# Optimization experiments

Hardware: AMD Instinct MI355X
Metric: run time of the kernel (lower is better)

The kernel has to match this reference:

```python
import jax, jax.numpy as jnp
import numpy as np
import math

B, A, IN_C, OUT_C = 64, 128, 128, 64

def _l2norm(x, eps=1e-12):
    # matches F.normalize(dim=1) on 2D input: x / max(||x||_2, eps) along last dim
    n = jnp.sqrt(jnp.sum(x * x, axis=-1, keepdims=True))
    return x / jnp.maximum(n, eps)

def setup_inputs() -> dict:
    key = jax.random.key(0)
    ks = jax.random.split(key, 7)
    s = 1.0 / math.sqrt(IN_C)
    return {
        "features": jax.random.normal(ks[0], (B, IN_C, A), dtype=jnp.float32),
        "Wq": jax.random.uniform(ks[1], (OUT_C, IN_C), jnp.float32, -s, s),
        "bq": jax.random.uniform(ks[2], (OUT_C,), jnp.float32, -s, s),
        "Wk": jax.random.uniform(ks[3], (OUT_C, IN_C), jnp.float32, -s, s),
        "bk": jax.random.uniform(ks[4], (OUT_C,), jnp.float32, -s, s),
        "Wv": jax.random.uniform(ks[5], (OUT_C, IN_C), jnp.float32, -s, s),
        "bv": jax.random.uniform(ks[6], (OUT_C,), jnp.float32, -s, s),
    }

def reference(features, Wq, bq, Wk, bk, Wv, bv):
    b = features.shape[0]
    f = jnp.transpose(features, (0, 2, 1))          # (b, a, in_c)
    a = f.shape[1]
    q = f @ Wq.T + bq                               # (b, a, d)
    k = f @ Wk.T + bk
    v = f @ Wv.T + bv
    d = q.shape[-1]
    qf = q.reshape(-1, d)                           # (N, d), N = b*a
    kf = k.reshape(-1, d)
    vf = v.reshape(-1, d)
    att = jax.nn.softmax(qf @ kf.T / math.sqrt(d), axis=1)  # (N, N)
    qkv = att @ vf                                  # (N, d)
    qkv_n = _l2norm(qkv).reshape(b, a, d)
    v_n = _l2norm(vf).reshape(b, a, d)
    # sim_s[i,j] = (1/a) * sum_t v_n[i,t] . qkv_n[j,t]  (diagonal-trace over 'a')
    sim_s = jnp.einsum('bad,cad->bc', v_n, qkv_n) / a
    return sim_s
```

## Files before the change

### kernel.cpp

```cpp
#include <hip/hip_runtime.h>
#include <hip/hip_bf16.h>

#define NROW 8192
#define INC  128
#define OUTC 64
#define BG   16

#define QSCALE 0.18033688011112042f

typedef __bf16 bf16x8 __attribute__((ext_vector_type(8)));
typedef __bf16 bf16x4 __attribute__((ext_vector_type(4)));
typedef short  s16x4  __attribute__((ext_vector_type(4)));
typedef float  f32x4  __attribute__((ext_vector_type(4)));

static __device__ __forceinline__ f32x4 mfma16(bf16x8 a, bf16x8 b, f32x4 c) {
    return __builtin_amdgcn_mfma_f32_16x16x32_bf16(a, b, c, 0, 0, 0);
}
static __device__ __forceinline__ f32x4 mfma1k(s16x4 a, s16x4 b, f32x4 c) {
    return __builtin_amdgcn_mfma_f32_16x16x16bf16_1k(a, b, c, 0, 0, 0);
}

static __device__ __forceinline__ bf16x8 cvt8(float4 lo, float4 hi) {
    bf16x8 r;
    r[0] = (__bf16)lo.x; r[1] = (__bf16)lo.y; r[2] = (__bf16)lo.z; r[3] = (__bf16)lo.w;
    r[4] = (__bf16)hi.x; r[5] = (__bf16)hi.y; r[6] = (__bf16)hi.z; r[7] = (__bf16)hi.w;
    return r;
}

__global__ __launch_bounds__(256) void proj_kernel(
    const float* __restrict__ feat,
    const float* __restrict__ Wq, const float* __restrict__ bq,
    const float* __restrict__ Wk, const float* __restrict__ bk,
    const float* __restrict__ Wv, const float* __restrict__ bv,
    __hip_bfloat16* __restrict__ qbf, __hip_bfloat16* __restrict__ kbf,
    __hip_bfloat16* __restrict__ vbf, __hip_bfloat16* __restrict__ vnb)
{
    __shared__ float slab[32 * 132];
    __shared__ float vbuf[32 * 66];
    __shared__ float invb[32];

    const int blk = blockIdx.x;
    const int b   = blk >> 2;
    const int a0  = (blk & 3) * 32;
    const int r0  = b * 128 + a0;
    const float* fb = feat + (size_t)b * INC * 128;

    for (int i = threadIdx.x; i < 32 * 128; i += 256) {
        int c = i >> 5, a = i & 31;
        slab[a * 132 + c] = fb[c * 128 + a0 + a];
    }
    __syncthreads();

    const int w    = threadIdx.x >> 6;
    const int lane = threadIdx.x & 63;
    const int l16  = lane & 15;
    const int quad = lane >> 4;

    f32x4 acc[3][2];
    #pragma unroll
    for (int t = 0; t < 3; ++t)
        #pragma unroll
        for (int u = 0; u < 2; ++u)
            acc[t][u] = (f32x4){0.f, 0.f, 0.f, 0.f};

    #pragma unroll
    for (int kc = 0; kc < 4; ++kc) {
        const int k0 = kc * 32 + quad * 8;
        bf16x8 afr[2];
        #pragma unroll
        for (int u = 0; u < 2; ++u) {
            const float* ar = slab + (u * 16 + l16) * 132 + k0;
            afr[u] = cvt8(*(const float4*)ar, *(const float4*)(ar + 4));
        }
        #pragma unroll
        for (int t = 0; t < 3; ++t) {
            const int tile = w * 3 + t;
            const int mat  = tile >> 2;
            const float* W = (mat == 0) ? Wq : (mat == 1) ? Wk : Wv;
            const float* wr = W + ((tile & 3) * 16 + l16) * INC + k0;
            bf16x8 bfr = cvt8(*(const float4*)wr, *(const float4*)(wr + 4));
            #pragma unroll
            for (int u = 0; u < 2; ++u)
                acc[t][u] = mfma16(afr[u], bfr, acc[t][u]);
        }
    }

    #pragma unroll
    for (int t = 0; t < 3; ++t) {
        const int tile = w * 3 + t;
        const int mat  = tile >> 2;
        const int nt   = tile & 3;
        const float* bias = (mat == 0) ? bq : (mat == 1) ? bk : bv;
        const float bl = bias[nt * 16 + l16];
        if (mat < 2) {
            const float sc = (mat == 0) ? QSCALE : 1.0f;
            __hip_bfloat16* dst = mat ? kbf : qbf;
            #pragma unroll
            for (int u = 0; u < 2; ++u) {
                const int base = ((((r0 >> 4) + u) * 4 + nt) << 8) + l16;
                #pragma unroll
                for (int r = 0; r < 4; ++r)
                    dst[base + (quad * 4 + r) * 16] = __float2bfloat16((acc[t][u][r] + bl) * sc);
            }
        } else {
            #pragma unroll
            for (int u = 0; u < 2; ++u)
                #pragma unroll
                for (int r = 0; r < 4; ++r)
                    vbuf[(u * 16 + quad * 4 + r) * 66 + nt * 16 + l16] = acc[t][u][r] + bl;
        }
    }
    __syncthreads();

    const int rl = threadIdx.x >> 3;
    const int jj = threadIdx.x & 7;
    float ss = 0.f;
    #pragma unroll
    for (int i = 0; i < 8; ++i) {
        float x = vbuf[rl * 66 + jj * 8 + i];
        ss += x * x;
    }
    ss += __shfl_xor(ss, 1, 64);
    ss += __shfl_xor(ss, 2, 64);
    ss += __shfl_xor(ss, 4, 64);
    if (jj == 0) invb[rl] = rsqrtf(fmaxf(ss, 1e-24f));
    __syncthreads();
    float inv = invb[rl];
    bf16x8 vp;
    #pragma unroll
    for (int i = 0; i < 8; ++i)
        vp[i] = (__bf16)(vbuf[rl * 66 + jj * 8 + i] * inv);
    *(bf16x8*)(vnb + (size_t)(r0 + rl) * 64 + jj * 8) = vp;
    const int tl = threadIdx.x & 15;
    const int n  = (threadIdx.x >> 4) & 3;
    const int s_ = threadIdx.x >> 6;
    bf16x8 pack;
    #pragma unroll
    for (int j = 0; j < 8; ++j) {
        int key = s_ * 8 + j;
        pack[j] = (__bf16)(vbuf[key * 66 + n * 16 + tl] * invb[key]);
    }
    const int base = ((((r0 >> 4) + (s_ >> 1)) * 4 + n) << 8) + tl * 16 + (s_ & 1) * 8;
    *(bf16x8*)(vbf + base) = pack;
}

#define ATTN_ITER(K00,K01,K10,K11, NK00,NK01,NK10,NK11,                      \
                  V0,V1,V2,V3,V4,V5,V6,V7,                                   \
                  NV0,NV1,NV2,NV3,NV4,NV5,NV6,NV7)                           \
    do {                                                                     \
        NV0 = *(const s16x4*)(vp);                                           \
        NV1 = *(const s16x4*)(vp + 512);                                     \
        NV2 = *(const s16x4*)(vp + 1024);                                    \
        NV3 = *(const s16x4*)(vp + 1536);                                    \
        NV4 = *(const s16x4*)(vp + 2048);                                    \
        NV5 = *(const s16x4*)(vp + 2560);                                    \
        NV6 = *(const s16x4*)(vp + 3072);                                    \
        NV7 = *(const s16x4*)(vp + 3584);                                    \
        NK00 = *(const bf16x8*)(kp);                                         \
        NK01 = *(const bf16x8*)(kp + 1024);                                  \
        NK10 = *(const bf16x8*)(kp + 2048);                                  \
        NK11 = *(const bf16x8*)(kp + 3072);                                  \
        vp += 4096; kp += 4096;                                              \
        const f32x4 zero = (f32x4){0.f, 0.f, 0.f, 0.f};                      \
        _Pragma("unroll")                                                    \
        for (int u = 0; u < 4; ++u) {                                        \
            f32x4 s0 = mfma16(K00, qf32[u][0], zero);                        \
            s0       = mfma16(K01, qf32[u][1], s0);                          \
            f32x4 s1 = mfma16(K10, qf32[u][0], zero);                        \
            s1       = mfma16(K11, qf32[u][1], s1);                          \
            union { bf16x4 v; s16x4 s; } pf0, pf1;                           \
            _Pragma("unroll")                                                \
            for (int r = 0; r < 4; ++r) {                                    \
                float p0 = __builtin_amdgcn_exp2f(s0[r]);                    \
                float p1 = __builtin_amdgcn_exp2f(s1[r]);                    \
                lp[u] += p0 + p1;                                            \
                pf0.v[r] = (__bf16)p0;                                       \
                pf1.v[r] = (__bf16)p1;                                       \
            }                                                                \
            of[u][0] = mfma1k(pf0.s, V0, of[u][0]);                          \
            of[u][0] = mfma1k(pf1.s, V4, of[u][0]);                          \
            of[u][1] = mfma1k(pf0.s, V1, of[u][1]);                          \
            of[u][1] = mfma1k(pf1.s, V5, of[u][1]);                          \
            of[u][2] = mfma1k(pf0.s, V2, of[u][2]);                          \
            of[u][2] = mfma1k(pf1.s, V6, of[u][2]);                          \
            of[u][3] = mfma1k(pf0.s, V3, of[u][3]);                          \
            of[u][3] = mfma1k(pf1.s, V7, of[u][3]);                          \
        }                                                                    \
    } while (0)

__global__ __launch_bounds__(256, 2) void attn_kernel(
    const __hip_bfloat16* __restrict__ qbf,
    const __hip_bfloat16* __restrict__ kbf,
    const __hip_bfloat16* __restrict__ vbf,
    float* __restrict__ Opart, float* __restrict__ lpart)
{
    const int qb    = blockIdx.x >> 4;
    const int bg    = blockIdx.x & 15;
    const int w     = threadIdx.x >> 6;
    const int lane  = threadIdx.x & 63;
    const int l16   = lane & 15;
    const int quad  = lane >> 4;
    const int r0    = qb * 256 + w * 64;
    const int fo    = l16 * 16 + quad * 4;
    const int fo32  = l16 * 16 + (quad & 1) * 8;
    const int qh    = quad >> 1;

    bf16x8 qf32[4][2];
    #pragma unroll
    for (int u = 0; u < 4; ++u)
        #pragma unroll
        for (int p = 0; p < 2; ++p)
            qf32[u][p] = *(const bf16x8*)(qbf +
                ((((r0 >> 4) + u) * 4 + p * 2 + qh) << 8) + fo32);

    f32x4 of[4][4];
    float lp[4] = {0.f, 0.f, 0.f, 0.f};
    #pragma unroll
    for (int u = 0; u < 4; ++u)
        #pragma unroll
        for (int n = 0; n < 4; ++n)
            of[u][n] = (f32x4){0.f, 0.f, 0.f, 0.f};

    const int ck0 = bg * 32;
    const char* kp = (const char*)kbf + ck0 * 2048 + qh * 512 + fo32 * 2;
    const char* vp = (const char*)vbf + ck0 * 2048 + fo * 2;

    bf16x8 kA00, kA01, kA10, kA11, kB00, kB01, kB10, kB11;
    s16x4  vA0, vA1, vA2, vA3, vA4, vA5, vA6, vA7;
    s16x4  vB0, vB1, vB2, vB3, vB4, vB5, vB6, vB7;

    vA0 = *(const s16x4*)(vp);
    vA1 = *(const s16x4*)(vp + 512);
    vA2 = *(const s16x4*)(vp + 1024);
    vA3 = *(const s16x4*)(vp + 1536);
    vA4 = *(const s16x4*)(vp + 2048);
    vA5 = *(const s16x4*)(vp + 2560);
    vA6 = *(const s16x4*)(vp + 3072);
    vA7 = *(const s16x4*)(vp + 3584);
    kA00 = *(const bf16x8*)(kp);
    kA01 = *(const bf16x8*)(kp + 1024);
    kA10 = *(const bf16x8*)(kp + 2048);
    kA11 = *(const bf16x8*)(kp + 3072);
    vp += 4096; kp += 4096;

    #pragma unroll 1
    for (int body = 0; body < 8; ++body) {
        ATTN_ITER(kA00, kA01, kA10, kA11, kB00, kB01, kB10, kB11,
                  vA0, vA1, vA2, vA3, vA4, vA5, vA6, vA7,
                  vB0, vB1, vB2, vB3, vB4, vB5, vB6, vB7);
        ATTN_ITER(kB00, kB01, kB10, kB11, kA00, kA01, kA10, kA11,
                  vB0, vB1, vB2, vB3, vB4, vB5, vB6, vB7,
                  vA0, vA1, vA2, vA3, vA4, vA5, vA6, vA7);
    }

    #pragma unroll
    for (int u = 0; u < 4; ++u) {
        float v = lp[u];
        v += __shfl_xor(v, 16, 64);
        v += __shfl_xor(v, 32, 64);
        lp[u] = v;
    }

    const int task = (qb * 4 + w) * 16 + bg;
    float* Ob = Opart + (size_t)task * 4096;
    #pragma unroll
    for (int u = 0; u < 4; ++u)
        #pragma unroll
        for (int n = 0; n < 4; ++n)
            #pragma unroll
            for (int r = 0; r < 4; ++r)
                Ob[(u * 16 + quad * 4 + r) * 64 + n * 16 + l16] = of[u][n][r];
    if (quad == 0) {
        #pragma unroll
        for (int u = 0; u < 4; ++u)
            lpart[task * 64 + u * 16 + l16] = lp[u];
    }
}

__global__ __launch_bounds__(256) void combine_kernel(
    const float* __restrict__ Opart, const float* __restrict__ lpart,
    __hip_bfloat16* __restrict__ qnb)
{
    const int r    = blockIdx.x * 4 + (threadIdx.x >> 6);
    const int c    = threadIdx.x & 63;
    const int tile = r >> 6, row = r & 63;
    float acc = 0.f, lsum = 0.f;
    #pragma unroll
    for (int g = 0; g < 16; ++g) {
        int task = tile * 16 + g;
        acc  += Opart[(size_t)task * 4096 + row * 64 + c];
        lsum += lpart[task * 64 + row];
    }
    float q = acc / lsum;
    float ss = q * q;
    ss += __shfl_xor(ss, 1, 64);
    ss += __shfl_xor(ss, 2, 64);
    ss += __shfl_xor(ss, 4, 64);
    ss += __shfl_xor(ss, 8, 64);
    ss += __shfl_xor(ss, 16, 64);
    ss += __shfl_xor(ss, 32, 64);
    qnb[(size_t)r * 64 + c] = __float2bfloat16(q * rsqrtf(fmaxf(ss, 1e-24f)));
}

__global__ __launch_bounds__(256) void sim_kernel(
    const __hip_bfloat16* __restrict__ vnb,
    const __hip_bfloat16* __restrict__ qnb,
    float* __restrict__ out)
{
    const int w    = threadIdx.x >> 6;
    const int lane = threadIdx.x & 63;
    const int l16  = lane & 15;
    const int quad = lane >> 4;
    const int kblk = blockIdx.x * 256;

    f32x4 acc[4][4];
    #pragma unroll
    for (int mi = 0; mi < 4; ++mi)
        #pragma unroll
        for (int ni = 0; ni < 4; ++ni)
            acc[mi][ni] = (f32x4){0.f, 0.f, 0.f, 0.f};

    #pragma unroll
    for (int s = 0; s < 2; ++s) {
        const int ks = w * 2 + s;
        const int k0 = kblk + ks * 32 + quad * 8;
        bf16x8 af[4], bfv[4];
        #pragma unroll
        for (int mi = 0; mi < 4; ++mi)
            af[mi] = *(const bf16x8*)(vnb + (size_t)(mi * 16 + l16) * 8192 + k0);
        #pragma unroll
        for (int ni = 0; ni < 4; ++ni)
            bfv[ni] = *(const bf16x8*)(qnb + (size_t)(ni * 16 + l16) * 8192 + k0);
        #pragma unroll
        for (int mi = 0; mi < 4; ++mi)
            #pragma unroll
            for (int ni = 0; ni < 4; ++ni)
                acc[mi][ni] = mfma16(af[mi], bfv[ni], acc[mi][ni]);
    }

    #pragma unroll
    for (int mi = 0; mi < 4; ++mi)
        #pragma unroll
        for (int ni = 0; ni < 4; ++ni)
            #pragma unroll
            for (int r = 0; r < 4; ++r)
                atomicAdd(&out[(mi * 16 + quad * 4 + r) * 64 + ni * 16 + l16],
                          acc[mi][ni][r] * (1.f / 128.f));
}

extern "C" void kernel_launch(void* const* d_in, const int* in_sizes, int n_in,
                              void* d_out, int out_size, void* d_ws, size_t ws_size,
                              hipStream_t stream)
{
    const float* feat = (const float*)d_in[0];
    const float* Wq   = (const float*)d_in[1];
    const float* bq   = (const float*)d_in[2];
    const float* Wk   = (const float*)d_in[3];
    const float* bk   = (const float*)d_in[4];
    const float* Wv   = (const float*)d_in[5];
    const float* bv   = (const float*)d_in[6];
    float* out = (float*)d_out;

    const size_t MB = 1u << 20;
    char* ws = (char*)d_ws;
    __hip_bfloat16* qbf = (__hip_bfloat16*)(ws);
    __hip_bfloat16* kbf = (__hip_bfloat16*)(ws + 1 * MB);
    __hip_bfloat16* vbf = (__hip_bfloat16*)(ws + 2 * MB);
    __hip_bfloat16* vnb = (__hip_bfloat16*)(ws + 3 * MB);
    float* Opart = (float*)(ws + 4 * MB);
    float* lpart = (float*)(ws + 36 * MB);
    __hip_bfloat16* qnb = (__hip_bfloat16*)(ws + 37 * MB);

    (void)hipMemsetAsync(out, 0, 64 * 64 * sizeof(float), stream);
    proj_kernel<<<256, 256, 0, stream>>>(feat, Wq, bq, Wk, bk, Wv, bv, qbf, kbf, vbf, vnb);
    attn_kernel<<<512, 256, 0, stream>>>(qbf, kbf, vbf, Opart, lpart);
    combine_kernel<<<2048, 256, 0, stream>>>(Opart, lpart, qnb);
    sim_kernel<<<32, 256, 0, stream>>>(vnb, qnb, out);
}
```

Baseline: 121.4 us.

## Widen V fragment loads, fold output zeroing into combine, split sim over more blocks

Changes the V tile layout written by the projection kernel so the attention kernel can fetch each lane's V fragments with four 16-byte loads instead of eight 8-byte loads, halving the load instruction count in the hot loop. Removes the separate hipMemsetAsync by zeroing the output inside the first block of the combine kernel. Doubles the number of sim_kernel blocks, each doing one K-step, to spread the final reduction across more CUs at the cost of twice as many atomic adds.

```diff
diff --git a/kernel.cpp b/kernel.cpp
--- a/kernel.cpp
+++ b/kernel.cpp
@@ -11,6 +11,7 @@
 typedef __bf16 bf16x8 __attribute__((ext_vector_type(8)));
 typedef __bf16 bf16x4 __attribute__((ext_vector_type(4)));
 typedef short  s16x4  __attribute__((ext_vector_type(4)));
+typedef short  s16x8  __attribute__((ext_vector_type(8)));
 typedef float  f32x4  __attribute__((ext_vector_type(4)));
 
 static __device__ __forceinline__ f32x4 mfma16(bf16x8 a, bf16x8 b, f32x4 c) {
@@ -25,6 +26,12 @@
     r[0] = (__bf16)lo.x; r[1] = (__bf16)lo.y; r[2] = (__bf16)lo.z; r[3] = (__bf16)lo.w;
     r[4] = (__bf16)hi.x; r[5] = (__bf16)hi.y; r[6] = (__bf16)hi.z; r[7] = (__bf16)hi.w;
     return r;
+}
+static __device__ __forceinline__ s16x4 vlo(s16x8 x) {
+    return __builtin_shufflevector(x, x, 0, 1, 2, 3);
+}
+static __device__ __forceinline__ s16x4 vhi(s16x8 x) {
+    return __builtin_shufflevector(x, x, 4, 5, 6, 7);
 }
 
 __global__ __launch_bounds__(256) void proj_kernel(
@@ -131,6 +138,7 @@
     for (int i = 0; i < 8; ++i)
         vp[i] = (__bf16)(vbuf[rl * 66 + jj * 8 + i] * inv);
     *(bf16x8*)(vnb + (size_t)(r0 + rl) * 64 + jj * 8) = vp;
+
     const int tl = threadIdx.x & 15;
     const int n  = (threadIdx.x >> 4) & 3;
     const int s_ = threadIdx.x >> 6;
@@ -140,22 +148,21 @@
         int key = s_ * 8 + j;
         pack[j] = (__bf16)(vbuf[key * 66 + n * 16 + tl] * invb[key]);
     }
-    const int base = ((((r0 >> 4) + (s_ >> 1)) * 4 + n) << 8) + tl * 16 + (s_ & 1) * 8;
-    *(bf16x8*)(vbf + base) = pack;
+    const int hblk = (r0 >> 4) + (s_ >> 1);
+    const int eb = hblk * 1024 + (n >> 1) * 512 + tl * 32 + (s_ & 1) * 16 + (n & 1) * 4;
+    bf16x4 plo = __builtin_shufflevector(pack, pack, 0, 1, 2, 3);
+    bf16x4 phi = __builtin_shufflevector(pack, pack, 4, 5, 6, 7);
+    *(bf16x4*)(vbf + eb)     = plo;
+    *(bf16x4*)(vbf + eb + 8) = phi;
 }
 
 #define ATTN_ITER(K00,K01,K10,K11, NK00,NK01,NK10,NK11,                      \
-                  V0,V1,V2,V3,V4,V5,V6,V7,                                   \
-                  NV0,NV1,NV2,NV3,NV4,NV5,NV6,NV7)                           \
+                  W0,W1,W2,W3, NW0,NW1,NW2,NW3)                              \
     do {                                                                     \
-        NV0 = *(const s16x4*)(vp);                                           \
-        NV1 = *(const s16x4*)(vp + 512);                                     \
-        NV2 = *(const s16x4*)(vp + 1024);                                    \
-        NV3 = *(const s16x4*)(vp + 1536);                                    \
-        NV4 = *(const s16x4*)(vp + 2048);                                    \
-        NV5 = *(const s16x4*)(vp + 2560);                                    \
-        NV6 = *(const s16x4*)(vp + 3072);                                    \
-        NV7 = *(const s16x4*)(vp + 3584);                                    \
+        NW0 = *(const s16x8*)(vp);                            \
+        NW1 = *(const s16x8*)(vp + 1024);                     \
+        NW2 = *(const s16x8*)(vp + 2048);                     \
+        NW3 = *(const s16x8*)(vp + 3072);                     \
         NK00 = *(const bf16x8*)(kp);                                         \
         NK01 = *(const bf16x8*)(kp + 1024);                                  \
         NK10 = *(const bf16x8*)(kp + 2048);                                  \
@@ -177,14 +184,14 @@
                 pf0.v[r] = (__bf16)p0;                                       \
                 pf1.v[r] = (__bf16)p1;                                       \
             }                                                                \
-            of[u][0] = mfma1k(pf0.s, V0, of[u][0]);                          \
-            of[u][0] = mfma1k(pf1.s, V4, of[u][0]);                          \
-            of[u][1] = mfma1k(pf0.s, V1, of[u][1]);                          \
-            of[u][1] = mfma1k(pf1.s, V5, of[u][1]);                          \
-            of[u][2] = mfma1k(pf0.s, V2, of[u][2]);                          \
-            of[u][2] = mfma1k(pf1.s, V6, of[u][2]);                          \
-            of[u][3] = mfma1k(pf0.s, V3, of[u][3]);                          \
-            of[u][3] = mfma1k(pf1.s, V7, of[u][3]);                          \
+            of[u][0] = mfma1k(pf0.s, vlo(W0), of[u][0]);                     \
+            of[u][0] = mfma1k(pf1.s, vlo(W2), of[u][0]);                     \
+            of[u][1] = mfma1k(pf0.s, vhi(W0), of[u][1]);                     \
+            of[u][1] = mfma1k(pf1.s, vhi(W2), of[u][1]);                     \
+            of[u][2] = mfma1k(pf0.s, vlo(W1), of[u][2]);                     \
+            of[u][2] = mfma1k(pf1.s, vlo(W3), of[u][2]);                     \
+            of[u][3] = mfma1k(pf0.s, vhi(W1), of[u][3]);                     \
+            of[u][3] = mfma1k(pf1.s, vhi(W3), of[u][3]);                     \
         }                                                                    \
     } while (0)
 
@@ -201,7 +208,6 @@
     const int l16   = lane & 15;
     const int quad  = lane >> 4;
     const int r0    = qb * 256 + w * 64;
-    const int fo    = l16 * 16 + quad * 4;
     const int fo32  = l16 * 16 + (quad & 1) * 8;
     const int qh    = quad >> 1;
 
@@ -223,20 +229,15 @@
 
     const int ck0 = bg * 32;
     const char* kp = (const char*)kbf + ck0 * 2048 + qh * 512 + fo32 * 2;
-    const char* vp = (const char*)vbf + ck0 * 2048 + fo * 2;
+    const char* vp = (const char*)vbf + ck0 * 2048 + l16 * 64 + quad * 16;
 
     bf16x8 kA00, kA01, kA10, kA11, kB00, kB01, kB10, kB11;
-    s16x4  vA0, vA1, vA2, vA3, vA4, vA5, vA6, vA7;
-    s16x4  vB0, vB1, vB2, vB3, vB4, vB5, vB6, vB7;
-
-    vA0 = *(const s16x4*)(vp);
-    vA1 = *(const s16x4*)(vp + 512);
-    vA2 = *(const s16x4*)(vp + 1024);
-    vA3 = *(const s16x4*)(vp + 1536);
-    vA4 = *(const s16x4*)(vp + 2048);
-    vA5 = *(const s16x4*)(vp + 2560);
-    vA6 = *(const s16x4*)(vp + 3072);
-    vA7 = *(const s16x4*)(vp + 3584);
+    s16x8  wA0, wA1, wA2, wA3, wB0, wB1, wB2, wB3;
+
+    wA0 = *(const s16x8*)(vp);
+    wA1 = *(const s16x8*)(vp + 1024);
+    wA2 = *(const s16x8*)(vp + 2048);
+    wA3 = *(const s16x8*)(vp + 3072);
     kA00 = *(const bf16x8*)(kp);
     kA01 = *(const bf16x8*)(kp + 1024);
     kA10 = *(const bf16x8*)(kp + 2048);
@@ -246,11 +247,9 @@
     #pragma unroll 1
     for (int body = 0; body < 8; ++body) {
         ATTN_ITER(kA00, kA01, kA10, kA11, kB00, kB01, kB10, kB11,
-                  vA0, vA1, vA2, vA3, vA4, vA5, vA6, vA7,
-                  vB0, vB1, vB2, vB3, vB4, vB5, vB6, vB7);
+                  wA0, wA1, wA2, wA3, wB0, wB1, wB2, wB3);
         ATTN_ITER(kB00, kB01, kB10, kB11, kA00, kA01, kA10, kA11,
-                  vB0, vB1, vB2, vB3, vB4, vB5, vB6, vB7,
-                  vA0, vA1, vA2, vA3, vA4, vA5, vA6, vA7);
+                  wB0, wB1, wB2, wB3, wA0, wA1, wA2, wA3);
     }
 
     #pragma unroll
@@ -279,8 +278,14 @@
 
 __global__ __launch_bounds__(256) void combine_kernel(
     const float* __restrict__ Opart, const float* __restrict__ lpart,
-    __hip_bfloat16* __restrict__ qnb)
-{
+    __hip_bfloat16* __restrict__ qnb, float* __restrict__ outz)
+{
+    if (blockIdx.x == 0) {
+        #pragma unroll
+        for (int z = 0; z < 4; ++z)
+            ((float4*)outz)[threadIdx.x * 4 + z] = (float4){0.f, 0.f, 0.f, 0.f};
+    }
+
     const int r    = blockIdx.x * 4 + (threadIdx.x >> 6);
     const int c    = threadIdx.x & 63;
     const int tile = r >> 6, row = r & 63;
@@ -311,7 +316,7 @@
     const int lane = threadIdx.x & 63;
     const int l16  = lane & 15;
     const int quad = lane >> 4;
-    const int kblk = blockIdx.x * 256;
+    const int k0   = blockIdx.x * 128 + w * 32 + quad * 8;
 
     f32x4 acc[4][4];
     #pragma unroll
@@ -320,23 +325,18 @@
         for (int ni = 0; ni < 4; ++ni)
             acc[mi][ni] = (f32x4){0.f, 0.f, 0.f, 0.f};
 
-    #pragma unroll
-    for (int s = 0; s < 2; ++s) {
-        const int ks = w * 2 + s;
-        const int k0 = kblk + ks * 32 + quad * 8;
-        bf16x8 af[4], bfv[4];
-        #pragma unroll
-        for (int mi = 0; mi < 4; ++mi)
-            af[mi] = *(const bf16x8*)(vnb + (size_t)(mi * 16 + l16) * 8192 + k0);
+    bf16x8 af[4], bfv[4];
+    #pragma unroll
+    for (int mi = 0; mi < 4; ++mi)
+        af[mi] = *(const bf16x8*)(vnb + (size_t)(mi * 16 + l16) * 8192 + k0);
+    #pragma unroll
+    for (int ni = 0; ni < 4; ++ni)
+        bfv[ni] = *(const bf16x8*)(qnb + (size_t)(ni * 16 + l16) * 8192 + k0);
+    #pragma unroll
+    for (int mi = 0; mi < 4; ++mi)
         #pragma unroll
         for (int ni = 0; ni < 4; ++ni)
-            bfv[ni] = *(const bf16x8*)(qnb + (size_t)(ni * 16 + l16) * 8192 + k0);
-        #pragma unroll
-        for (int mi = 0; mi < 4; ++mi)
-            #pragma unroll
-            for (int ni = 0; ni < 4; ++ni)
-                acc[mi][ni] = mfma16(af[mi], bfv[ni], acc[mi][ni]);
-    }
+            acc[mi][ni] = mfma16(af[mi], bfv[ni], acc[mi][ni]);
 
     #pragma unroll
     for (int mi = 0; mi < 4; ++mi)
@@ -371,9 +371,8 @@
     float* lpart = (float*)(ws + 36 * MB);
     __hip_bfloat16* qnb = (__hip_bfloat16*)(ws + 37 * MB);
 
-    (void)hipMemsetAsync(out, 0, 64 * 64 * sizeof(float), stream);
     proj_kernel<<<256, 256, 0, stream>>>(feat, Wq, bq, Wk, bk, Wv, bv, qbf, kbf, vbf, vnb);
     attn_kernel<<<512, 256, 0, stream>>>(qbf, kbf, vbf, Opart, lpart);
-    combine_kernel<<<2048, 256, 0, stream>>>(Opart, lpart, qnb);
-    sim_kernel<<<32, 256, 0, stream>>>(vnb, qnb, out);
-}
+    combine_kernel<<<2048, 256, 0, stream>>>(Opart, lpart, qnb, out);
+    sim_kernel<<<64, 256, 0, stream>>>(vnb, qnb, out);
+}
```

Result: no change. 123.1 us (+1.4%).
